# Kernel tuning notes

Measured on AMD Instinct MI355X. Metric: run time of the kernel, lower is better.

## Reference

```python
import jax, jax.numpy as jnp
import numpy as np

D_MODEL = 512
WINDOW_SIZE = 257


def setup_inputs() -> dict:
    key = jax.random.key(0)
    ks = jax.random.split(key, 7)
    B, S, D = 4, 4096, D_MODEL
    scale = 1.0 / np.sqrt(D)
    return {
        "x": jax.random.normal(ks[0], (B, S, D), dtype=jnp.float32),
        "Wq": jax.random.normal(ks[1], (D, D), dtype=jnp.float32) * scale,
        "bq": jnp.zeros((D,), dtype=jnp.float32),
        "Wk": jax.random.normal(ks[2], (D, D), dtype=jnp.float32) * scale,
        "bk": jnp.zeros((D,), dtype=jnp.float32),
        "Wv": jax.random.normal(ks[3], (D, D), dtype=jnp.float32) * scale,
        "bv": jnp.zeros((D,), dtype=jnp.float32),
    }


def reference(x, Wq, bq, Wk, bk, Wv, bv):
    B, S, D = x.shape
    half_window = (WINDOW_SIZE - 1) // 2
    Q = x @ Wq + bq
    K = x @ Wk + bk
    V = x @ Wv + bv
    # full [B,S,S] scores, then band mask |i-j| <= half_window (matches original)
    scores = jnp.einsum("bsd,btd->bst", Q, K) / jnp.sqrt(jnp.asarray(D, x.dtype))
    idx = jnp.arange(S)
    local_mask = jnp.abs(idx[:, None] - idx[None, :]) <= half_window  # [S,S]
    scores = jnp.where(local_mask[None], scores, -jnp.inf)
    attn = jax.nn.softmax(scores, axis=-1)
    return jnp.einsum("bst,btd->bsd", attn, V)
```

## Files before the change

kernel.cpp:

```cpp
#include <hip/hip_runtime.h>
#include <hip/hip_bf16.h>

#define S_LEN   4096
#define D_MOD   512
#define BATCH   4
#define HALF_W  128
#define M_TOT   (BATCH * S_LEN)

typedef __attribute__((ext_vector_type(8))) short bf16x8;
typedef __attribute__((ext_vector_type(4))) float f32x4;

__device__ __forceinline__ unsigned short f2bf(float f) {
    unsigned int u = __float_as_uint(f);
    unsigned int r = (u + 0x7fffu + ((u >> 16) & 1u)) >> 16;
    return (unsigned short)r;
}

__device__ __forceinline__ void async_copy16(const void* g, void* l) {
    __builtin_amdgcn_global_load_lds(
        (const __attribute__((address_space(1))) void*)g,
        (__attribute__((address_space(3))) void*)l, 16, 0, 0);
}

__global__ __launch_bounds__(256) void convert_xw(const float* __restrict__ x,
                                                  const float* __restrict__ Wq,
                                                  const float* __restrict__ Wk,
                                                  const float* __restrict__ Wv,
                                                  unsigned short* __restrict__ xb,
                                                  unsigned short* __restrict__ Wt) {
    __shared__ float sT[64][65];
    const int t = threadIdx.x;
    const int bid = blockIdx.x;
    if (bid < 8192) {
        int i = (bid * 256 + t) * 4;
        float4 v = *(const float4*)(x + i);
        ushort4 o;
        o.x = f2bf(v.x); o.y = f2bf(v.y); o.z = f2bf(v.z); o.w = f2bf(v.w);
        *(ushort4*)(xb + i) = o;
        return;
    }
    const int j = bid - 8192;
    const int w = j >> 6;
    const int rj = j & 63;
    const float* W = (w == 0) ? Wq : ((w == 1) ? Wk : Wv);
    const int n0 = (rj & 7) * 64, k0 = (rj >> 3) * 64;
    const int r = t >> 4, c4 = (t & 15) * 4;
    #pragma unroll
    for (int i = 0; i < 4; ++i) {
        float4 v = *(const float4*)(W + (size_t)(k0 + r + i * 16) * 512 + n0 + c4);
        sT[c4 + 0][r + i * 16] = v.x;
        sT[c4 + 1][r + i * 16] = v.y;
        sT[c4 + 2][r + i * 16] = v.z;
        sT[c4 + 3][r + i * 16] = v.w;
    }
    __syncthreads();
    #pragma unroll
    for (int i = 0; i < 4; ++i) {
        int rr = (t >> 4) + i * 16;
        ushort4 o;
        o.x = f2bf(sT[rr][c4 + 0]);
        o.y = f2bf(sT[rr][c4 + 1]);
        o.z = f2bf(sT[rr][c4 + 2]);
        o.w = f2bf(sT[rr][c4 + 3]);
        *(ushort4*)(Wt + (size_t)w * 262144 + (size_t)(n0 + rr) * 512 + k0 + c4) = o;
    }
}

__global__ __launch_bounds__(256) void qkv_gemm(
    const unsigned short* __restrict__ xb, const unsigned short* __restrict__ Wt,
    const float* __restrict__ bq, const float* __restrict__ bk, const float* __restrict__ bv,
    unsigned short* __restrict__ Qo, unsigned short* __restrict__ Ko,
    unsigned short* __restrict__ Vt) {
    __shared__ __align__(16) char gsmem[34816];
    unsigned short* sA = (unsigned short*)gsmem;
    unsigned short* sB = (unsigned short*)(gsmem + 16384);
    unsigned short* sT = (unsigned short*)gsmem;

    const int t = threadIdx.x;
    const int p = blockIdx.x;
    const int l = (p & 7) * 192 + (p >> 3);
    const int mi = l / 12;
    const int rzn = l - mi * 12;
    const int wsel = rzn >> 2;
    const int ni = rzn & 3;
    const int m0 = mi * 128;
    const int n0 = ni * 128;
    const unsigned short* Wb = Wt + (size_t)wsel * 262144;

    const int w = t >> 6, lane = t & 63;
    const int wm = (w & 1) * 64, wn = (w >> 1) * 64;
    const int qd = lane >> 4, l16 = lane & 15;

    f32x4 acc[4][4] = {};

    for (int k0 = 0; k0 < 512; k0 += 64) {
        __syncthreads();
        #pragma unroll
        for (int i = 0; i < 4; ++i) {
            int c = i * 256 + t;
            int row = c >> 3, cc = c & 7;
            int g = cc ^ (row & 7);
            async_copy16(xb + (size_t)(m0 + row) * 512 + k0 + g * 8, sA + c * 8);
            async_copy16(Wb + (size_t)(n0 + row) * 512 + k0 + g * 8, sB + c * 8);
        }
        __syncthreads();
        #pragma unroll
        for (int ks = 0; ks < 2; ++ks) {
            bf16x8 af[4], bfr[4];
            #pragma unroll
            for (int i = 0; i < 4; ++i) {
                int row = wm + i * 16 + l16;
                int ch = (ks * 4 + qd) ^ (row & 7);
                af[i] = *(const bf16x8*)(sA + row * 64 + ch * 8);
            }
            #pragma unroll
            for (int j = 0; j < 4; ++j) {
                int row = wn + j * 16 + l16;
                int ch = (ks * 4 + qd) ^ (row & 7);
                bfr[j] = *(const bf16x8*)(sB + row * 64 + ch * 8);
            }
            #pragma unroll
            for (int i = 0; i < 4; ++i)
                #pragma unroll
                for (int j = 0; j < 4; ++j)
                    acc[i][j] = __builtin_amdgcn_mfma_f32_16x16x32_bf16(af[i], bfr[j], acc[i][j], 0, 0, 0);
        }
    }

    const float* bias = (wsel == 0) ? bq : ((wsel == 1) ? bk : bv);
    __syncthreads();

    if (wsel < 2) {
        #pragma unroll
        for (int j = 0; j < 4; ++j) {
            int n = wn + j * 16 + l16;
            float bj = bias[n0 + n];
            #pragma unroll
            for (int i = 0; i < 4; ++i) {
                int mb = wm + i * 16 + qd * 4;
                #pragma unroll
                for (int r = 0; r < 4; ++r)
                    sT[(mb + r) * 136 + n] = f2bf(acc[i][j][r] + bj);
            }
        }
        __syncthreads();
        unsigned short* Og = (wsel == 0) ? Qo : Ko;
        #pragma unroll
        for (int i2 = 0; i2 < 4; ++i2)
            #pragma unroll
            for (int i3 = 0; i3 < 2; ++i3) {
                int m = i2 * 32 + (t >> 3);
                int ch = (t & 7) + i3 * 8;
                bf16x8 v = *(const bf16x8*)(sT + m * 136 + ch * 8);
                *(bf16x8*)(Og + (size_t)(m0 + m) * 512 + n0 + ch * 8) = v;
            }
    } else {
        #pragma unroll
        for (int j = 0; j < 4; ++j) {
            int n = wn + j * 16 + l16;
            float bj = bias[n0 + n];
            #pragma unroll
            for (int i = 0; i < 4; ++i) {
                int mb = wm + i * 16 + qd * 4;
                #pragma unroll
                for (int r = 0; r < 4; ++r)
                    sT[n * 136 + mb + r] = f2bf(acc[i][j][r] + bj);
            }
        }
        __syncthreads();
        #pragma unroll
        for (int i2 = 0; i2 < 4; ++i2)
            #pragma unroll
            for (int i3 = 0; i3 < 2; ++i3) {
                int n = i2 * 32 + (t >> 3);
                int ch = (t & 7) + i3 * 8;
                bf16x8 v = *(const bf16x8*)(sT + n * 136 + ch * 8);
                *(bf16x8*)(Vt + (size_t)(n0 + n) * M_TOT + m0 + ch * 8) = v;
            }
    }
}

__global__ __launch_bounds__(256) void attn(const unsigned short* __restrict__ Qg,
                                            const unsigned short* __restrict__ Kg,
                                            const unsigned short* __restrict__ Vt,
                                            float* __restrict__ out) {
    __shared__ __align__(16) unsigned short sQ[32 * 520];
    __shared__ __align__(16) unsigned short sKV[32 * 520];
    __shared__ __align__(16) unsigned short sP[32 * 40];
    __shared__ float lsum[32];

    const int t = threadIdx.x;
    const int p = blockIdx.x;
    const int l = (p & 7) * 64 + (p >> 3);
    const int q0 = (l & 127) * 32;
    const int b = l >> 7;
    const int bS = b * S_LEN;
    const int w = t >> 6, lane = t & 63;
    const int qd = lane >> 4, l16 = lane & 15;
    const int qh = (w >> 1) * 16, kh = (w & 1) * 16;

    if (t < 32) lsum[t] = 0.f;

    #pragma unroll
    for (int i = 0; i < 8; ++i) {
        int c = i * 256 + t;
        int row = c >> 6, cc = c & 63;
        async_copy16(Qg + (bS + q0 + row) * 512 + cc * 8, sQ + row * 520 + cc * 8);
    }

    f32x4 oacc[16] = {};

    for (int kt = 0; kt < 9; ++kt) {
        int key0 = q0 - HALF_W + kt * 32;
        if (key0 + 32 <= 0 || key0 >= S_LEN) continue;

        __syncthreads();
        #pragma unroll
        for (int i = 0; i < 8; ++i) {
            int c = i * 256 + t;
            int row = c >> 6, cc = c & 63;
            int rowg = key0 + row;
            rowg = (rowg < 0) ? 0 : ((rowg > S_LEN - 1) ? S_LEN - 1 : rowg);
            async_copy16(Kg + (bS + rowg) * 512 + cc * 8, sKV + row * 520 + cc * 8);
        }
        __syncthreads();

        f32x4 sacc = {0.f, 0.f, 0.f, 0.f};
        #pragma unroll
        for (int c4 = 0; c4 < 4; ++c4) {
            #pragma unroll
            for (int kc = 0; kc < 4; ++kc) {
                bf16x8 aq = *(const bf16x8*)(sQ + (qh + l16) * 520 + c4 * 128 + kc * 32 + qd * 8);
                bf16x8 bk8 = *(const bf16x8*)(sKV + (kh + l16) * 520 + c4 * 128 + kc * 32 + qd * 8);
                sacc = __builtin_amdgcn_mfma_f32_16x16x32_bf16(aq, bk8, sacc, 0, 0, 0);
            }
        }

        const float scale = 0.04419417382415922f;
        #pragma unroll
        for (int r = 0; r < 4; ++r) {
            int qi = q0 + qh + qd * 4 + r;
            int kj = key0 + kh + l16;
            bool valid = (kj >= 0) && (kj < S_LEN) && (kj >= qi - HALF_W) && (kj <= qi + HALF_W);
            float p2 = valid ? __expf(sacc[r] * scale) : 0.f;
            sP[(qh + qd * 4 + r) * 40 + kh + l16] = f2bf(p2);
            float s = p2;
            s += __shfl_xor(s, 1);
            s += __shfl_xor(s, 2);
            s += __shfl_xor(s, 4);
            s += __shfl_xor(s, 8);
            if (l16 == 0) atomicAdd(&lsum[qh + qd * 4 + r], s);
        }

        __syncthreads();
        #pragma unroll
        for (int i = 0; i < 8; ++i) {
            int c = i * 256 + t;
            int row = c >> 2, cc = c & 3;
            int kk = key0 + cc * 8;
            int koff = (kk >= 0 && kk + 8 <= S_LEN) ? kk : 0;
            async_copy16(Vt + (size_t)row * M_TOT + bS + koff, sKV + c * 8);
        }
        __syncthreads();

        #pragma unroll
        for (int c4 = 0; c4 < 4; ++c4) {
            #pragma unroll
            for (int qt = 0; qt < 2; ++qt) {
                bf16x8 ap = *(const bf16x8*)(sP + (qt * 16 + l16) * 40 + qd * 8);
                #pragma unroll
                for (int dt = 0; dt < 2; ++dt) {
                    bf16x8 bv8 = *(const bf16x8*)(sKV + (c4 * 128 + w * 32 + dt * 16 + l16) * 32 + qd * 8);
                    oacc[c4 * 4 + qt * 2 + dt] =
                        __builtin_amdgcn_mfma_f32_16x16x32_bf16(ap, bv8, oacc[c4 * 4 + qt * 2 + dt], 0, 0, 0);
                }
            }
        }
    }

    __syncthreads();
    #pragma unroll
    for (int c4 = 0; c4 < 4; ++c4)
        #pragma unroll
        for (int qt = 0; qt < 2; ++qt)
            #pragma unroll
            for (int dt = 0; dt < 2; ++dt) {
                int dv = c4 * 128 + w * 32 + dt * 16 + l16;
                #pragma unroll
                for (int r = 0; r < 4; ++r) {
                    int q = qt * 16 + qd * 4 + r;
                    out[(size_t)(bS + q0 + q) * 512 + dv] = oacc[c4 * 4 + qt * 2 + dt][r] / lsum[q];
                }
            }
}

extern "C" void kernel_launch(void* const* d_in, const int* in_sizes, int n_in,
                              void* d_out, int out_size, void* d_ws, size_t ws_size,
                              hipStream_t stream) {
    const float* x  = (const float*)d_in[0];
    const float* Wq = (const float*)d_in[1];
    const float* bq = (const float*)d_in[2];
    const float* Wk = (const float*)d_in[3];
    const float* bk = (const float*)d_in[4];
    const float* Wv = (const float*)d_in[5];
    const float* bv = (const float*)d_in[6];
    float* out = (float*)d_out;

    char* ws = (char*)d_ws;
    unsigned short* xb = (unsigned short*)(ws);
    unsigned short* Wt = (unsigned short*)(ws + 16777216);
    unsigned short* Qb = (unsigned short*)(ws + 18350080);
    unsigned short* Kb = (unsigned short*)(ws + 35127296);
    unsigned short* Vt = (unsigned short*)(ws + 51904512);

    convert_xw<<<8384, 256, 0, stream>>>(x, Wq, Wk, Wv, xb, Wt);
    qkv_gemm<<<1536, 256, 0, stream>>>(xb, Wt, bq, bk, bv, Qb, Kb, Vt);
    attn<<<512, 256, 0, stream>>>(Qb, Kb, Vt, out);
}
```

Baseline: 167.2 us.

## Keep Q in registers and split K/V LDS buffers to overlap staging

Q fragments now stay in registers for the whole block instead of being staged through LDS. K and V get separate shared buffers, so the V tile load is issued before the QK^T MFMAs and the next K tile is prefetched during the PV MFMAs, which removes two barriers per iteration. The key-tile loop bounds are computed up front rather than skipping inside the loop. The aim is to hide global-to-LDS latency behind matrix work, at the cost of roughly 64 extra VGPRs per thread, which may lower occupancy.

Result: slower. 174.3 us (+4.3%).

```diff
diff --git a/kernel.cpp b/kernel.cpp
--- a/kernel.cpp
+++ b/kernel.cpp
@@ -184,8 +184,8 @@
                                             const unsigned short* __restrict__ Kg,
                                             const unsigned short* __restrict__ Vt,
                                             float* __restrict__ out) {
-    __shared__ __align__(16) unsigned short sQ[32 * 520];
-    __shared__ __align__(16) unsigned short sKV[32 * 520];
+    __shared__ __align__(16) unsigned short sK[32 * 520];
+    __shared__ __align__(16) unsigned short sV[512 * 32];
     __shared__ __align__(16) unsigned short sP[32 * 40];
     __shared__ float lsum[32];
 
@@ -201,38 +201,56 @@
 
     if (t < 32) lsum[t] = 0.f;
 
-    #pragma unroll
-    for (int i = 0; i < 8; ++i) {
-        int c = i * 256 + t;
-        int row = c >> 6, cc = c & 63;
-        async_copy16(Qg + (bS + q0 + row) * 512 + cc * 8, sQ + row * 520 + cc * 8);
+    bf16x8 qf[16];
+    {
+        const unsigned short* qrow = Qg + (size_t)(bS + q0 + qh + l16) * 512 + qd * 8;
+        #pragma unroll
+        for (int kc = 0; kc < 16; ++kc) qf[kc] = *(const bf16x8*)(qrow + kc * 32);
     }
 
     f32x4 oacc[16] = {};
 
-    for (int kt = 0; kt < 9; ++kt) {
-        int key0 = q0 - HALF_W + kt * 32;
-        if (key0 + 32 <= 0 || key0 >= S_LEN) continue;
-
-        __syncthreads();
+    auto stageK = [&](int key0) {
         #pragma unroll
         for (int i = 0; i < 8; ++i) {
             int c = i * 256 + t;
             int row = c >> 6, cc = c & 63;
             int rowg = key0 + row;
             rowg = (rowg < 0) ? 0 : ((rowg > S_LEN - 1) ? S_LEN - 1 : rowg);
-            async_copy16(Kg + (bS + rowg) * 512 + cc * 8, sKV + row * 520 + cc * 8);
-        }
-        __syncthreads();
+            async_copy16(Kg + (size_t)(bS + rowg) * 512 + cc * 8, sK + row * 520 + cc * 8);
+        }
+    };
+    auto stageV = [&](int key0) {
+        #pragma unroll
+        for (int i = 0; i < 8; ++i) {
+            int c = i * 256 + t;
+            int row = c >> 2, cc = c & 3;
+            int kk = key0 + cc * 8;
+            int koff = (kk >= 0 && kk + 8 <= S_LEN) ? kk : 0;
+            async_copy16(Vt + (size_t)row * M_TOT + bS + koff, sV + c * 8);
+        }
+    };
+
+    const int ti = q0 >> 5;
+    const int kt_lo = (4 - ti) > 0 ? (4 - ti) : 0;
+    const int kh_t = (4192 - q0) >> 5;
+    const int kt_hi = kh_t < 8 ? kh_t : 8;
+
+    stageK(q0 - HALF_W + kt_lo * 32);
+
+    for (int kt = kt_lo; kt <= kt_hi; ++kt) {
+        int key0 = q0 - HALF_W + kt * 32;
+
+        __syncthreads();
+        stageV(key0);
 
         f32x4 sacc = {0.f, 0.f, 0.f, 0.f};
         #pragma unroll
         for (int c4 = 0; c4 < 4; ++c4) {
             #pragma unroll
             for (int kc = 0; kc < 4; ++kc) {
-                bf16x8 aq = *(const bf16x8*)(sQ + (qh + l16) * 520 + c4 * 128 + kc * 32 + qd * 8);
-                bf16x8 bk8 = *(const bf16x8*)(sKV + (kh + l16) * 520 + c4 * 128 + kc * 32 + qd * 8);
-                sacc = __builtin_amdgcn_mfma_f32_16x16x32_bf16(aq, bk8, sacc, 0, 0, 0);
+                bf16x8 bk8 = *(const bf16x8*)(sK + (kh + l16) * 520 + c4 * 128 + kc * 32 + qd * 8);
+                sacc = __builtin_amdgcn_mfma_f32_16x16x32_bf16(qf[c4 * 4 + kc], bk8, sacc, 0, 0, 0);
             }
         }
 
@@ -253,15 +271,7 @@
         }
 
         __syncthreads();
-        #pragma unroll
-        for (int i = 0; i < 8; ++i) {
-            int c = i * 256 + t;
-            int row = c >> 2, cc = c & 3;
-            int kk = key0 + cc * 8;
-            int koff = (kk >= 0 && kk + 8 <= S_LEN) ? kk : 0;
-            async_copy16(Vt + (size_t)row * M_TOT + bS + koff, sKV + c * 8);
-        }
-        __syncthreads();
+        if (kt < kt_hi) stageK(key0 + 32);
 
         #pragma unroll
         for (int c4 = 0; c4 < 4; ++c4) {
@@ -270,7 +280,7 @@
                 bf16x8 ap = *(const bf16x8*)(sP + (qt * 16 + l16) * 40 + qd * 8);
                 #pragma unroll
                 for (int dt = 0; dt < 2; ++dt) {
-                    bf16x8 bv8 = *(const bf16x8*)(sKV + (c4 * 128 + w * 32 + dt * 16 + l16) * 32 + qd * 8);
+                    bf16x8 bv8 = *(const bf16x8*)(sV + (c4 * 128 + w * 32 + dt * 16 + l16) * 32 + qd * 8);
                     oacc[c4 * 4 + qt * 2 + dt] =
                         __builtin_amdgcn_mfma_f32_16x16x32_bf16(ap, bv8, oacc[c4 * 4 + qt * 2 + dt], 0, 0, 0);
                 }
@@ -278,7 +288,6 @@
         }
     }
 
-    __syncthreads();
     #pragma unroll
     for (int c4 = 0; c4 < 4; ++c4)
         #pragma unroll
```
